# Performance work log

Measured on AMD Instinct MI355X. Metric: run time of the kernel, lower is better.

Reference implementation:

```python
import jax, jax.numpy as jnp
import numpy as np

D_MODEL = 768
N_HEADS = 12
D_HEAD = D_MODEL // N_HEADS
B, T = 2, 4096


def setup_inputs() -> dict:
    key = jax.random.key(0)
    ks = jax.random.split(key, 9)
    s = 1.0 / np.sqrt(D_MODEL)
    x = jax.random.normal(ks[0], (B, T, D_MODEL), dtype=jnp.float32)
    Wq = jax.random.uniform(ks[1], (D_MODEL, D_MODEL), jnp.float32, -s, s)
    Wk = jax.random.uniform(ks[2], (D_MODEL, D_MODEL), jnp.float32, -s, s)
    Wv = jax.random.uniform(ks[3], (D_MODEL, D_MODEL), jnp.float32, -s, s)
    Wo = jax.random.uniform(ks[4], (D_MODEL, D_MODEL), jnp.float32, -s, s)
    bq = jax.random.uniform(ks[5], (D_MODEL,), jnp.float32, -s, s)
    bk = jax.random.uniform(ks[6], (D_MODEL,), jnp.float32, -s, s)
    bv = jax.random.uniform(ks[7], (D_MODEL,), jnp.float32, -s, s)
    bo = jax.random.uniform(ks[8], (D_MODEL,), jnp.float32, -s, s)
    return {"x": x, "Wq": Wq, "bq": bq, "Wk": Wk, "bk": bk,
            "Wv": Wv, "bv": bv, "Wo": Wo, "bo": bo}


def _split_heads(t):
    # [B, T, D] -> [B, H, T, d_head]
    Bc, Tc, _ = t.shape
    return t.reshape(Bc, Tc, N_HEADS, D_HEAD).transpose(0, 2, 1, 3)


def reference(x, Wq, bq, Wk, bk, Wv, bv, Wo, bo):
    scale = D_HEAD ** -0.5
    Q = _split_heads(x @ Wq.T + bq)
    K = _split_heads(x @ Wk.T + bk)
    V = _split_heads(x @ Wv.T + bv)
    scores = jnp.einsum('bhqd,bhkd->bhqk', Q, K) * scale  # [B,H,T,T]
    attn = jax.nn.softmax(scores, axis=-1)
    out = jnp.einsum('bhqk,bhkd->bhqd', attn, V)  # [B,H,T,d_head]
    out = out.transpose(0, 2, 1, 3).reshape(x.shape[0], x.shape[1], D_MODEL)
    return out @ Wo.T + bo
```

## Files before the change

kernel.cpp:

```cpp
#include <hip/hip_runtime.h>
#include <hip/hip_bf16.h>

#define DM 768
#define NH 12
#define TB 2
#define TT 4096
#define MM (TB*TT)
#define NQKV (3*DM)
#define NW (DM*DM)
#define NX (MM*DM)
#define CEQ 0.18033688f

typedef unsigned short u16;
typedef short s16x8 __attribute__((ext_vector_type(8)));
typedef unsigned short u16x8 __attribute__((ext_vector_type(8)));
typedef float f32x4 __attribute__((ext_vector_type(4)));
typedef float f32x16 __attribute__((ext_vector_type(16)));
typedef unsigned u32x4 __attribute__((ext_vector_type(4)));

#if __has_builtin(__builtin_amdgcn_exp2f)
#define EXP2 __builtin_amdgcn_exp2f
#else
#define EXP2 exp2f
#endif

__device__ __forceinline__ u16 f2bf(float f) {
  unsigned u = __builtin_bit_cast(unsigned, f);
  unsigned r = (u + 0x7FFFu + ((u >> 16) & 1u)) >> 16;
  return (u16)r;
}

__device__ __forceinline__ unsigned cvtpk(float lo, float hi) {
  unsigned r;
  asm("v_cvt_pk_bf16_f32 %0, %1, %2" : "=v"(r) : "v"(lo), "v"(hi));
  return r;
}

__device__ __forceinline__ void gload16(const void* g, void* l) {
  __builtin_amdgcn_global_load_lds(
      (const __attribute__((address_space(1))) void*)g,
      (__attribute__((address_space(3))) void*)l, 16, 0, 0);
}

__device__ __forceinline__ void plswap(unsigned a, unsigned b, unsigned& r0, unsigned& r1) {
#if __has_builtin(__builtin_amdgcn_permlane32_swap)
  auto rr = __builtin_amdgcn_permlane32_swap(a, b, false, false);
  unsigned tmp[2];
  __builtin_memcpy(tmp, &rr, 8);
  r0 = tmp[0]; r1 = tmp[1];
#else
  int hi_ = (threadIdx.x >> 5) & 1;
  unsigned bx = (unsigned)__shfl_xor((int)b, 32, 64);
  unsigned ax = (unsigned)__shfl_xor((int)a, 32, 64);
  r0 = hi_ ? bx : a;
  r1 = hi_ ? b : ax;
#endif
}

__device__ __forceinline__ float xhalf_sum(float v) {
  unsigned a = __builtin_bit_cast(unsigned, v), r0, r1;
  plswap(a, a, r0, r1);
  return __builtin_bit_cast(float, r0) + __builtin_bit_cast(float, r1);
}

__device__ __forceinline__ void repack2(const f32x16& sv, s16x8& fa, s16x8& fb) {
  {
    unsigned cA0 = cvtpk(sv[0], sv[1]),  cA1 = cvtpk(sv[2], sv[3]);
    unsigned cB0 = cvtpk(sv[4], sv[5]),  cB1 = cvtpk(sv[6], sv[7]);
    unsigned w0, w1, w2, w3;
    plswap(cA0, cB0, w0, w2);
    plswap(cA1, cB1, w1, w3);
    u32x4 w = {w0, w1, w2, w3};
    fa = __builtin_bit_cast(s16x8, w);
  }
  {
    unsigned cA0 = cvtpk(sv[8], sv[9]),   cA1 = cvtpk(sv[10], sv[11]);
    unsigned cB0 = cvtpk(sv[12], sv[13]), cB1 = cvtpk(sv[14], sv[15]);
    unsigned w0, w1, w2, w3;
    plswap(cA0, cB0, w0, w2);
    plswap(cA1, cB1, w1, w3);
    u32x4 w = {w0, w1, w2, w3};
    fb = __builtin_bit_cast(s16x8, w);
  }
}

__global__ __launch_bounds__(256) void cast_prep(
    const float* __restrict__ x, const float* __restrict__ wq,
    const float* __restrict__ wk, const float* __restrict__ wv,
    const float* __restrict__ wo, const float* __restrict__ bq,
    const float* __restrict__ bk, const float* __restrict__ bv,
    u16* __restrict__ xb, u16* __restrict__ wqkvb, u16* __restrict__ wob,
    float* __restrict__ bqkv) {
  int g = blockIdx.x * 256 + threadIdx.x;
  int e = g * 4;
  const float* src;
  u16* dst;
  if (e < NX) { src = x + e; dst = xb + e; }
  else {
    int e2 = e - NX;
    if (e2 < 3*NW) {
      const float* w = (e2 < NW) ? wq : (e2 < 2*NW ? wk : wv);
      int base = (e2 < NW) ? 0 : (e2 < 2*NW ? NW : 2*NW);
      src = w + (e2 - base); dst = wqkvb + e2;
    } else { int e3 = e2 - 3*NW; src = wo + e3; dst = wob + e3; }
  }
  float4 v = *(const float4*)src;
  ushort4 p;
  p.x = f2bf(v.x); p.y = f2bf(v.y); p.z = f2bf(v.z); p.w = f2bf(v.w);
  *(ushort4*)dst = p;
  if (blockIdx.x == 0) {
    for (int i = threadIdx.x; i < NQKV; i += 256)
      bqkv[i] = (i < DM) ? bq[i] : (i < 2*DM ? bk[i-DM] : bv[i-2*DM]);
  }
}

__global__ __launch_bounds__(256, 3) void gemm_qkv(
    const u16* __restrict__ A, const u16* __restrict__ W,
    const float* __restrict__ bias,
    u16* __restrict__ qb, u16* __restrict__ kb, u16* __restrict__ vt) {
  __shared__ __align__(16) u16 As[2][128*32], Bs[2][128*32];
  const int tid = threadIdx.x, lane = tid & 63, wave = tid >> 6;
  const int rg = lane & 15, cg = lane >> 4;
  int lin = blockIdx.y * 18 + blockIdx.x;
  int swz = (lin & 7) * 144 + (lin >> 3);
  const int m0 = (swz / 18) * 128, n0 = (swz % 18) * 128;
  const int wm = (wave >> 1) * 64, wn = (wave & 1) * 64;
  f32x4 acc[4][4];
#pragma unroll
  for (int i = 0; i < 4; i++)
#pragma unroll
    for (int j = 0; j < 4; j++) acc[i][j] = (f32x4){0.f,0.f,0.f,0.f};

  const u16* ga = A + (size_t)(m0 + (tid >> 2)) * DM + (tid & 3) * 8;
  const u16* gb = W + (size_t)(n0 + (tid >> 2)) * DM + (tid & 3) * 8;
  auto stage = [&](int kt, int buf) {
    int ko = kt * 32;
    char* la = (char*)&As[buf][0] + wave * 1024;
    char* lb = (char*)&Bs[buf][0] + wave * 1024;
    gload16(ga + ko,                    la);
    gload16(ga + (size_t)64*DM + ko,    la + 4096);
    gload16(gb + ko,                    lb);
    gload16(gb + (size_t)64*DM + ko,    lb + 4096);
  };

  stage(0, 0);
  __syncthreads();
  const int NT = DM / 32;
  int cur = 0;
  for (int kt = 0; kt < NT; ++kt) {
    if (kt + 1 < NT) stage(kt + 1, cur ^ 1);
    s16x8 af[4], bfv[4];
#pragma unroll
    for (int i = 0; i < 4; i++) af[i]  = *(const s16x8*)&As[cur][(wm + i*16 + rg)*32 + cg*8];
#pragma unroll
    for (int i = 0; i < 4; i++) bfv[i] = *(const s16x8*)&Bs[cur][(wn + i*16 + rg)*32 + cg*8];
    __builtin_amdgcn_s_setprio(1);
#pragma unroll
    for (int mi = 0; mi < 4; mi++)
#pragma unroll
      for (int ni = 0; ni < 4; ni++)
        acc[mi][ni] = __builtin_amdgcn_mfma_f32_16x16x32_bf16(af[mi], bfv[ni], acc[mi][ni], 0, 0, 0);
    __builtin_amdgcn_s_setprio(0);
    __syncthreads();
    cur ^= 1;
  }

#pragma unroll
  for (int ni = 0; ni < 4; ni++) {
    int o = n0 + wn + ni*16 + rg;
    float bia = bias[o];
    int mat = o / DM, d = o % DM;
    int head = d >> 6, dh = d & 63;
    if (mat == 2) {
#pragma unroll
      for (int mi = 0; mi < 4; mi++) {
        int m = m0 + wm + mi*16 + cg*4;
        int b = m >> 12, t = m & 4095;
        ushort4 pv;
        pv.x = f2bf(acc[mi][ni][0] + bia);
        pv.y = f2bf(acc[mi][ni][1] + bia);
        pv.z = f2bf(acc[mi][ni][2] + bia);
        pv.w = f2bf(acc[mi][ni][3] + bia);
        *(ushort4*)&vt[((size_t)((b*NH + head)*64 + dh))*TT + t] = pv;
      }
    } else {
      u16* outp = mat ? kb : qb;
      float sc = mat ? 1.0f : CEQ;
#pragma unroll
      for (int mi = 0; mi < 4; mi++) {
#pragma unroll
        for (int r = 0; r < 4; r++) {
          int m = m0 + wm + mi*16 + cg*4 + r;
          int b = m >> 12, t = m & 4095;
          outp[((size_t)((b*NH + head)*TT + t))*64 + dh] = f2bf((acc[mi][ni][r] + bia) * sc);
        }
      }
    }
  }
}

__global__ __launch_bounds__(256, 3) void attn7(
    const u16* __restrict__ qg, const u16* __restrict__ kg,
    const u16* __restrict__ vtg, u16* __restrict__ h) {
  __shared__ __align__(16) char smem[49152];
  const int tid = threadIdx.x, lane = tid & 63, wave = tid >> 6;
  const int ql = lane & 31, hi = lane >> 5;
  int lin = blockIdx.y * 32 + blockIdx.x;
  int swz = (lin & 7) * 96 + (lin >> 3);
  int qt = swz & 31, bh = swz >> 5;
  const int b = bh / NH, head = bh % NH;
  const size_t hb = (size_t)bh * TT * 64;

  const int qrow = qt * 128 + wave * 32 + ql;
  const u16* qp = qg + hb + (size_t)qrow * 64 + hi * 8;
  s16x8 qf[4];
#pragma unroll
  for (int ds = 0; ds < 4; ++ds) qf[ds] = *(const s16x8*)(qp + ds * 16);

  const int lr = lane >> 3;
  const int lc = ((lane & 7) ^ lr) * 16;
  const char* kSrc = (const char*)(kg + hb) + lr * 128 + lc;
  const char* vSrc = (const char*)(vtg + hb) + (size_t)lr * 8192 + lc;
  auto stage = [&](int kt, int buf) {
    char* lk = smem + buf * 16384 + wave * 2048;
    char* lv = lk + 8192;
    const char* gk = kSrc + (size_t)kt * 8192 + wave * 2048;
    const char* gv = vSrc + (size_t)kt * 128 + (size_t)wave * 131072;
    gload16(gk,          lk);
    gload16(gk + 1024,   lk + 1024);
    gload16(gv,          lv);
    gload16(gv + 65536,  lv + 1024);
  };

  f32x16 o0 = {}, o1 = {};
  float L = 0.f;
  const int swb = (ql & 7) << 4;

  stage(0, 0);
  stage(1, 1);
  asm volatile("s_waitcnt vmcnt(4)" ::: "memory");
  __builtin_amdgcn_s_barrier();

  const int NKT = TT / 64;
  int cur = 0;
  for (int kt = 0; kt < NKT; ++kt) {
    int nb = cur + 2; if (nb >= 3) nb -= 3;
    if (kt + 2 < NKT) stage(kt + 2, nb);

    const char* bk_ = smem + cur * 16384 + ql * 128;
    const char* bv_ = bk_ + 8192;

    s16x8 kf0[4], kf1[4], vf0[4], vf1[4];
#pragma unroll
    for (int ds = 0; ds < 4; ++ds) {
      kf0[ds] = *(const s16x8*)(bk_ +        ((ds*32 + hi*16) ^ swb));
      kf1[ds] = *(const s16x8*)(bk_ + 4096 + ((ds*32 + hi*16) ^ swb));
    }
#pragma unroll
    for (int ks = 0; ks < 4; ++ks) {
      vf0[ks] = *(const s16x8*)(bv_ +        ((ks*32 + hi*16) ^ swb));
      vf1[ks] = *(const s16x8*)(bv_ + 4096 + ((ks*32 + hi*16) ^ swb));
    }

    f32x16 s0 = {}, s1 = {};
    __builtin_amdgcn_s_setprio(1);
#pragma unroll
    for (int ds = 0; ds < 4; ++ds) {
      s0 = __builtin_amdgcn_mfma_f32_32x32x16_bf16(kf0[ds], qf[ds], s0, 0, 0, 0);
      s1 = __builtin_amdgcn_mfma_f32_32x32x16_bf16(kf1[ds], qf[ds], s1, 0, 0, 0);
    }
    __builtin_amdgcn_s_setprio(0);

#pragma unroll
    for (int i = 0; i < 16; ++i) s0[i] = EXP2(s0[i]);
#pragma unroll
    for (int i = 0; i < 16; ++i) s1[i] = EXP2(s1[i]);
    f32x16 u = s0 + s1;
    float a0 = u[0] + u[8],  a1 = u[1] + u[9],  a2 = u[2] + u[10], a3 = u[3] + u[11];
    float a4 = u[4] + u[12], a5 = u[5] + u[13], a6 = u[6] + u[14], a7 = u[7] + u[15];
    a0 += a4; a1 += a5; a2 += a6; a3 += a7;
    a0 += a2; a1 += a3;
    L += a0 + a1;

    s16x8 pf[4];
    repack2(s0, pf[0], pf[1]);
    repack2(s1, pf[2], pf[3]);

    __builtin_amdgcn_s_setprio(1);
#pragma unroll
    for (int ks = 0; ks < 4; ++ks) {
      o0 = __builtin_amdgcn_mfma_f32_32x32x16_bf16(vf0[ks], pf[ks], o0, 0, 0, 0);
      o1 = __builtin_amdgcn_mfma_f32_32x32x16_bf16(vf1[ks], pf[ks], o1, 0, 0, 0);
    }
    __builtin_amdgcn_s_setprio(0);

    if (kt + 2 < NKT) {
      asm volatile("s_waitcnt vmcnt(4)" ::: "memory");
    } else {
      asm volatile("s_waitcnt vmcnt(0)" ::: "memory");
    }
    __builtin_amdgcn_s_barrier();
    cur = (cur == 2) ? 0 : cur + 1;
  }

  float Lt = xhalf_sum(L);
  float inv = 1.f / Lt;
  u16 (*ot)[32][72] = (u16(*)[32][72])smem;
#pragma unroll
  for (int db = 0; db < 2; ++db) {
    const f32x16& ov = db ? o1 : o0;
#pragma unroll
    for (int i = 0; i < 8; ++i) {
      unsigned w = cvtpk(ov[2*i] * inv, ov[2*i+1] * inv);
      int d = db*32 + ((2*i) & 3) + 8*((2*i) >> 2) + 4*hi;
      *(unsigned*)&ot[wave][ql][d] = w;
    }
  }
  __syncthreads();
  const u16* rowp = &ot[wave][ql][hi*32];
  u32x4 r0 = *(const u32x4*)(rowp);
  u32x4 r1 = *(const u32x4*)(rowp + 8);
  u32x4 r2 = *(const u32x4*)(rowp + 16);
  u32x4 r3 = *(const u32x4*)(rowp + 24);
  u16* dst = h + (size_t)(b*TT + qrow) * DM + head*64 + hi*32;
  *(u32x4*)(dst)      = r0;
  *(u32x4*)(dst + 8)  = r1;
  *(u32x4*)(dst + 16) = r2;
  *(u32x4*)(dst + 24) = r3;
}

__global__ __launch_bounds__(256, 3) void gemm_proj(
    const u16* __restrict__ A, const u16* __restrict__ W,
    const float* __restrict__ bias, float* __restrict__ out) {
  __shared__ __align__(16) u16 As[2][128*32], Bs[2][128*32];
  const int tid = threadIdx.x, lane = tid & 63, wave = tid >> 6;
  const int rg = lane & 15, cg = lane >> 4;
  int lin = blockIdx.y * 6 + blockIdx.x;
  int swz = (lin & 7) * 48 + (lin >> 3);
  const int m0 = (swz / 6) * 128, n0 = (swz % 6) * 128;
  const int wm = (wave >> 1) * 64, wn = (wave & 1) * 64;
  f32x4 acc[4][4];
#pragma unroll
  for (int i = 0; i < 4; i++)
#pragma unroll
    for (int j = 0; j < 4; j++) acc[i][j] = (f32x4){0.f,0.f,0.f,0.f};

  const u16* ga = A + (size_t)(m0 + (tid >> 2)) * DM + (tid & 3) * 8;
  const u16* gb = W + (size_t)(n0 + (tid >> 2)) * DM + (tid & 3) * 8;
  auto stage = [&](int kt, int buf) {
    int ko = kt * 32;
    char* la = (char*)&As[buf][0] + wave * 1024;
    char* lb = (char*)&Bs[buf][0] + wave * 1024;
    gload16(ga + ko,                    la);
    gload16(ga + (size_t)64*DM + ko,    la + 4096);
    gload16(gb + ko,                    lb);
    gload16(gb + (size_t)64*DM + ko,    lb + 4096);
  };

  stage(0, 0);
  __syncthreads();
  const int NT = DM / 32;
  int cur = 0;
  for (int kt = 0; kt < NT; ++kt) {
    if (kt + 1 < NT) stage(kt + 1, cur ^ 1);
    s16x8 af[4], bfv[4];
#pragma unroll
    for (int i = 0; i < 4; i++) af[i]  = *(const s16x8*)&As[cur][(wm + i*16 + rg)*32 + cg*8];
#pragma unroll
    for (int i = 0; i < 4; i++) bfv[i] = *(const s16x8*)&Bs[cur][(wn + i*16 + rg)*32 + cg*8];
    __builtin_amdgcn_s_setprio(1);
#pragma unroll
    for (int mi = 0; mi < 4; mi++)
#pragma unroll
      for (int ni = 0; ni < 4; ni++)
        acc[mi][ni] = __builtin_amdgcn_mfma_f32_16x16x32_bf16(af[mi], bfv[ni], acc[mi][ni], 0, 0, 0);
    __builtin_amdgcn_s_setprio(0);
    __syncthreads();
    cur ^= 1;
  }
#pragma unroll
  for (int ni = 0; ni < 4; ni++) {
    int o = n0 + wn + ni*16 + rg;
    float bia = bias[o];
#pragma unroll
    for (int mi = 0; mi < 4; mi++) {
#pragma unroll
      for (int r = 0; r < 4; r++) {
        int m = m0 + wm + mi*16 + cg*4 + r;
        out[(size_t)m * DM + o] = acc[mi][ni][r] + bia;
      }
    }
  }
}

extern "C" void kernel_launch(void* const* d_in, const int* in_sizes, int n_in,
                              void* d_out, int out_size, void* d_ws, size_t ws_size,
                              hipStream_t stream) {
  (void)in_sizes; (void)n_in; (void)out_size; (void)ws_size;
  const float* x  = (const float*)d_in[0];
  const float* Wq = (const float*)d_in[1];
  const float* bq = (const float*)d_in[2];
  const float* Wk = (const float*)d_in[3];
  const float* bk = (const float*)d_in[4];
  const float* Wv = (const float*)d_in[5];
  const float* bv = (const float*)d_in[6];
  const float* Wo = (const float*)d_in[7];
  const float* bo = (const float*)d_in[8];
  float* out = (float*)d_out;

  char* ws = (char*)d_ws;
  size_t off = 0;
  auto alloc = [&](size_t bytes) {
    char* p = ws + off;
    off = (off + bytes + 255) & ~(size_t)255;
    return p;
  };
  u16*   xb    = (u16*)alloc((size_t)NX * 2);
  u16*   wqkvb = (u16*)alloc((size_t)3 * NW * 2);
  u16*   wob   = (u16*)alloc((size_t)NW * 2);
  float* bqkv  = (float*)alloc((size_t)NQKV * 4);
  u16*   qb    = (u16*)alloc((size_t)NX * 2);
  u16*   kb    = (u16*)alloc((size_t)NX * 2);
  u16*   vtb   = (u16*)alloc((size_t)NX * 2);
  u16*   hbuf  = xb;

  cast_prep<<<(NX + 4*NW) / 4 / 256, 256, 0, stream>>>(x, Wq, Wk, Wv, Wo, bq, bk, bv,
                                                       xb, wqkvb, wob, bqkv);
  gemm_qkv<<<dim3(18, 64), 256, 0, stream>>>(xb, wqkvb, bqkv, qb, kb, vtb);
  attn7<<<dim3(32, TB*NH), 256, 0, stream>>>(qb, kb, vtb, hbuf);
  gemm_proj<<<dim3(6, 64), 256, 0, stream>>>(hbuf, wob, bo, out);
}
```

Before: 197.0 us.

## Software-pipeline attention loop: compute next tile's QK^T before current softmax/PV

The attention kernel's key-tile loop is restructured so the QK^T MFMAs for tile j+1 are issued before the exp2, row-sum and PV work of tile j. It uses ping-pong score accumulators and unrolls the loop by two. The goal is to overlap the VALU exponent work with matrix-core work, which were serialized inside each iteration before. Each stage now waits only for the K half of the following tile (vmcnt lowered from 4 to 2), so the early QK^T has its data in time. The extra pair of live 16-float accumulators raises register pressure under the 3-blocks-per-CU launch bound, which could cause spills or lower occupancy.

Result: slower. 702.4 us (+256.6%).

```diff
diff --git a/kernel.cpp b/kernel.cpp
--- a/kernel.cpp
+++ b/kernel.cpp
@@ -199,7 +199,7 @@
   }
 }
 
-__global__ __launch_bounds__(256, 3) void attn7(
+__global__ __launch_bounds__(256, 3) void attn8(
     const u16* __restrict__ qg, const u16* __restrict__ kg,
     const u16* __restrict__ vtg, u16* __restrict__ h) {
   __shared__ __align__(16) char smem[49152];
@@ -235,47 +235,69 @@
   f32x16 o0 = {}, o1 = {};
   float L = 0.f;
   const int swb = (ql & 7) << 4;
+  const int NKT = TT / 64;
 
   stage(0, 0);
   stage(1, 1);
-  asm volatile("s_waitcnt vmcnt(4)" ::: "memory");
+  asm volatile("s_waitcnt vmcnt(2)" ::: "memory");
   __builtin_amdgcn_s_barrier();
 
-  const int NKT = TT / 64;
-  int cur = 0;
-  for (int kt = 0; kt < NKT; ++kt) {
-    int nb = cur + 2; if (nb >= 3) nb -= 3;
-    if (kt + 2 < NKT) stage(kt + 2, nb);
-
-    const char* bk_ = smem + cur * 16384 + ql * 128;
-    const char* bv_ = bk_ + 8192;
-
-    s16x8 kf0[4], kf1[4], vf0[4], vf1[4];
+  f32x16 sA0, sA1, sB0, sB1;
+  {
+    const char* bk_ = smem + ql * 128;
+    s16x8 kf0[4], kf1[4];
 #pragma unroll
     for (int ds = 0; ds < 4; ++ds) {
       kf0[ds] = *(const s16x8*)(bk_ +        ((ds*32 + hi*16) ^ swb));
       kf1[ds] = *(const s16x8*)(bk_ + 4096 + ((ds*32 + hi*16) ^ swb));
     }
+    sA0 = (f32x16){}; sA1 = (f32x16){};
+    __builtin_amdgcn_s_setprio(1);
+#pragma unroll
+    for (int ds = 0; ds < 4; ++ds) {
+      sA0 = __builtin_amdgcn_mfma_f32_32x32x16_bf16(kf0[ds], qf[ds], sA0, 0, 0, 0);
+      sA1 = __builtin_amdgcn_mfma_f32_32x32x16_bf16(kf1[ds], qf[ds], sA1, 0, 0, 0);
+    }
+    __builtin_amdgcn_s_setprio(0);
+  }
+
+  int cur = 0;
+  auto body = [&](int j, f32x16& c0, f32x16& c1, f32x16& n0, f32x16& n1) {
+    int sb = cur + 2; if (sb >= 3) sb -= 3;
+    if (j + 2 < NKT) stage(j + 2, sb);
+    int nx = cur + 1; if (nx >= 3) nx -= 3;
+
+    const char* bv_ = smem + cur * 16384 + 8192 + ql * 128;
+    s16x8 vf0[4], vf1[4];
 #pragma unroll
     for (int ks = 0; ks < 4; ++ks) {
       vf0[ks] = *(const s16x8*)(bv_ +        ((ks*32 + hi*16) ^ swb));
       vf1[ks] = *(const s16x8*)(bv_ + 4096 + ((ks*32 + hi*16) ^ swb));
     }
 
-    f32x16 s0 = {}, s1 = {};
-    __builtin_amdgcn_s_setprio(1);
-#pragma unroll
-    for (int ds = 0; ds < 4; ++ds) {
-      s0 = __builtin_amdgcn_mfma_f32_32x32x16_bf16(kf0[ds], qf[ds], s0, 0, 0, 0);
-      s1 = __builtin_amdgcn_mfma_f32_32x32x16_bf16(kf1[ds], qf[ds], s1, 0, 0, 0);
-    }
-    __builtin_amdgcn_s_setprio(0);
-
-#pragma unroll
-    for (int i = 0; i < 16; ++i) s0[i] = EXP2(s0[i]);
-#pragma unroll
-    for (int i = 0; i < 16; ++i) s1[i] = EXP2(s1[i]);
-    f32x16 u = s0 + s1;
+    if (j + 1 < NKT) {
+      const char* bk_ = smem + nx * 16384 + ql * 128;
+      s16x8 kf0[4], kf1[4];
+#pragma unroll
+      for (int ds = 0; ds < 4; ++ds) {
+        kf0[ds] = *(const s16x8*)(bk_ +        ((ds*32 + hi*16) ^ swb));
+        kf1[ds] = *(const s16x8*)(bk_ + 4096 + ((ds*32 + hi*16) ^ swb));
+      }
+      n0 = (f32x16){}; n1 = (f32x16){};
+      __builtin_amdgcn_s_setprio(1);
+#pragma unroll
+      for (int ds = 0; ds < 4; ++ds) {
+        n0 = __builtin_amdgcn_mfma_f32_32x32x16_bf16(kf0[ds], qf[ds], n0, 0, 0, 0);
+        n1 = __builtin_amdgcn_mfma_f32_32x32x16_bf16(kf1[ds], qf[ds], n1, 0, 0, 0);
+      }
+      __builtin_amdgcn_s_setprio(0);
+    }
+
+#pragma unroll
+    for (int i = 0; i < 16; ++i) c0[i] = EXP2(c0[i]);
+#pragma unroll
+    for (int i = 0; i < 16; ++i) c1[i] = EXP2(c1[i]);
+    f32x16 u = c0 + c1;
     float a0 = u[0] + u[8],  a1 = u[1] + u[9],  a2 = u[2] + u[10], a3 = u[3] + u[11];
     float a4 = u[4] + u[12], a5 = u[5] + u[13], a6 = u[6] + u[14], a7 = u[7] + u[15];
     a0 += a4; a1 += a5; a2 += a6; a3 += a7;
@@ -283,8 +305,8 @@
     L += a0 + a1;
 
     s16x8 pf[4];
-    repack2(s0, pf[0], pf[1]);
-    repack2(s1, pf[2], pf[3]);
+    repack2(c0, pf[0], pf[1]);
+    repack2(c1, pf[2], pf[3]);
 
     __builtin_amdgcn_s_setprio(1);
 #pragma unroll
@@ -294,13 +316,18 @@
     }
     __builtin_amdgcn_s_setprio(0);
 
-    if (kt + 2 < NKT) {
-      asm volatile("s_waitcnt vmcnt(4)" ::: "memory");
+    if (j + 2 < NKT) {
+      asm volatile("s_waitcnt vmcnt(2)" ::: "memory");
     } else {
       asm volatile("s_waitcnt vmcnt(0)" ::: "memory");
     }
     __builtin_amdgcn_s_barrier();
-    cur = (cur == 2) ? 0 : cur + 1;
+    cur = nx;
+  };
+
+  for (int j = 0; j < NKT; j += 2) {
+    body(j,     sA0, sA1, sB0, sB1);
+    body(j + 1, sB0, sB1, sA0, sA1);
   }
 
   float Lt = xhalf_sum(L);
@@ -427,6 +454,6 @@
   cast_prep<<<(NX + 4*NW) / 4 / 256, 256, 0, stream>>>(x, Wq, Wk, Wv, Wo, bq, bk, bv,
                                                        xb, wqkvb, wob, bqkv);
   gemm_qkv<<<dim3(18, 64), 256, 0, stream>>>(xb, wqkvb, bqkv, qb, kb, vtb);
-  attn7<<<dim3(32, TB*NH), 256, 0, stream>>>(qb, kb, vtb, hbuf);
+  attn8<<<dim3(32, TB*NH), 256, 0, stream>>>(qb, kb, vtb, hbuf);
   gemm_proj<<<dim3(6, 64), 256, 0, stream>>>(hbuf, wob, bo, out);
 }
```
